# Optimization experiments

Measured on AMD Instinct MI355X. Metric: run time of the kernel, lower is better.

## Reference

```python
import jax, jax.numpy as jnp
import numpy as np

BATCH, SEQ, D_IN = 4, 2048, 1024
STATE, D_OUT, KX = 1024, 1024, 10


def setup_inputs() -> dict:
    key = jax.random.key(0)
    k0, k1, k2, k3, k4, k5 = jax.random.split(key, 6)
    inputs = jax.random.normal(k0, (BATCH, SEQ, D_IN), jnp.float32)
    h0 = jax.random.normal(k1, (STATE,), jnp.float32)
    A = jax.random.normal(k2, (STATE,), jnp.float32)
    A = A / jnp.max(jnp.abs(A))  # matches init_A / max|init_A|
    B = jax.random.normal(k3, (D_IN, STATE), jnp.float32) / D_IN
    C = jax.random.normal(k4, (STATE, D_OUT), jnp.float32) / STATE
    M = jax.random.normal(k5, (D_IN, D_OUT, KX), jnp.float32) / D_OUT
    return {"inputs": inputs, "h0": h0, "A": A, "B": B, "C": C, "M": M}


def compute_ar_x_preds(w, x):
    # w: (d_out, d_in, k); x: (b, l, d_in)
    d_out, d_in, k = w.shape
    b, l, _ = x.shape
    o = jnp.einsum('oik,bli->bklo', w, x)  # (b, k, l, d_out)
    shifts = jnp.arange(k)
    # roll slice i forward by i along the length axis
    o = jax.vmap(lambda oi, s: jnp.roll(oi, s, axis=1), in_axes=(1, 0), out_axes=1)(o, shifts)
    # triu mask: keep position t in slice i only if t >= i (causal AR)
    m = (jnp.arange(l)[None, :] >= shifts[:, None]).astype(o.dtype)  # (k, l)
    return jnp.sum(o * m[None, :, :, None], axis=1)  # (b, l, d_out)


def reference(inputs, h0, A, B, C, M):
    bsz = inputs.shape[0]
    h_init = jnp.broadcast_to(h0, (bsz, h0.shape[0]))  # h0.expand(bsz, state_dim)
    u_seq = jnp.swapaxes(inputs, 0, 1)  # (l, b, d_in)

    def step(h, u):
        h_new = A * h + u @ B  # diagonal recurrence
        return h_new, h_new

    _, hs = jax.lax.scan(step, h_init, u_seq)  # (l, b, state)
    all_h_t = jnp.swapaxes(hs, 0, 1)  # (b, l, state)
    lds_out = all_h_t @ C  # (b, l, d_out)
    ar = compute_ar_x_preds(M, inputs)
    return lds_out + ar
```

## Files before the change

### kernel.cpp

```cpp
#include <hip/hip_runtime.h>
#include <stdint.h>

typedef unsigned short u16;
typedef __attribute__((ext_vector_type(4))) float f32x4;
typedef __attribute__((ext_vector_type(8))) short s16x8;

#define BATCH 4
#define SEQ   2048
#define DIM   1024
#define KX    10
#define PAD   16
#define SEQP  (SEQ+PAD)

__device__ __forceinline__ u16 f2b(float f) {
    union { float f; uint32_t u; } v; v.f = f;
    uint32_t u = v.u + 0x7fffu + ((v.u >> 16) & 1u);
    return (u16)(u >> 16);
}
__device__ __forceinline__ float b2f(u16 h) {
    union { uint32_t u; float f; } v; v.u = ((uint32_t)h) << 16;
    return v.f;
}

__device__ __forceinline__ void llds16(const u16* g, u16* l) {
    __builtin_amdgcn_global_load_lds(
        (const __attribute__((address_space(1))) uint32_t*)g,
        (__attribute__((address_space(3))) uint32_t*)l, 16, 0, 0);
}

#define PREP_X_END  8256
#define PREP_C_END  10304
#define PREP_M_END  14400

__global__ __launch_bounds__(256) void k_prep(
    const float* __restrict__ x, const float* __restrict__ B,
    const float* __restrict__ C, const float* __restrict__ M,
    u16* __restrict__ Xpad, u16* __restrict__ Btr, u16* __restrict__ Wall)
{
    __shared__ float tile[32][33];
    const int bid = blockIdx.x, tid = threadIdx.x;

    if (bid < PREP_X_END) {
        int idx = bid * 256 + tid;
        long e = (long)idx * 4;
        int i = (int)(e & 1023);
        int row = (int)(e >> 10);
        int t = row % SEQP;
        int b = row / SEQP;
        ushort4 o;
        if (t < PAD) {
            o.x = 0; o.y = 0; o.z = 0; o.w = 0;
        } else {
            const float4 v = *(const float4*)(x + (((long)(b * SEQ + (t - PAD)) << 10) + i));
            o.x = f2b(v.x); o.y = f2b(v.y); o.z = f2b(v.z); o.w = f2b(v.w);
        }
        *(ushort4*)(Xpad + ((long)row << 10) + i) = o;
    } else if (bid < PREP_C_END) {
        const int tb = bid - PREP_X_END;
        const float* in = (tb < 1024) ? B : C;
        u16* out = (tb < 1024) ? Btr : Wall;
        int lb = tb & 1023;
        int bx = lb & 31, by = lb >> 5;
        int tx = tid & 31, ty = tid >> 5;
#pragma unroll
        for (int j = 0; j < 4; j++)
            tile[ty + j * 8][tx] = in[(long)(by * 32 + ty + j * 8) * 1024 + bx * 32 + tx];
        __syncthreads();
#pragma unroll
        for (int j = 0; j < 4; j++)
            out[(long)(bx * 32 + ty + j * 8) * 1024 + by * 32 + tx] = f2b(tile[tx][ty + j * 8]);
    } else {
        int idx = (bid - PREP_C_END) * 256 + tid;
        int o = idx >> 10, i = idx & 1023;
        const float* src = M + (long)idx * KX;
#pragma unroll
        for (int k = 0; k < KX; k++)
            Wall[((long)(k + 1) << 20) + ((long)o << 10) + i] = f2b(src[k]);
    }
}


__global__ void k_scan1(const u16* __restrict__ U, const float* __restrict__ A,
                        float* __restrict__ F) {
    int s = blockIdx.x * 256 + threadIdx.x;
    int bc = blockIdx.y;
    int b = bc >> 4, c = bc & 15;
    float a = A[s];
    const u16* u = U + (((long)(b * SEQ + c * 128)) << 10) + s;
    float f = 0.f;
#pragma unroll 8
    for (int j = 0; j < 128; j++) f = fmaf(a, f, b2f(u[(long)j << 10]));
    F[((long)bc << 10) + s] = f;
}

__global__ void k_scan2(const float* __restrict__ F, const float* __restrict__ A,
                        const float* __restrict__ h0, float* __restrict__ Carry) {
    int idx = blockIdx.x * 256 + threadIdx.x;
    int b = idx >> 10, s = idx & 1023;
    float a = A[s];
    float a128 = a;
#pragma unroll
    for (int q = 0; q < 7; q++) a128 *= a128;
    float carry = h0[s];
#pragma unroll
    for (int c = 0; c < 16; c++) {
        long off = ((long)(b * 16 + c) << 10) + s;
        Carry[off] = carry;
        carry = fmaf(a128, carry, F[off]);
    }
}

__global__ void k_scan3(u16* __restrict__ U, const float* __restrict__ A,
                        const float* __restrict__ Carry) {
    int s = blockIdx.x * 256 + threadIdx.x;
    int bc = blockIdx.y;
    int b = bc >> 4, c = bc & 15;
    float a = A[s];
    long base = (((long)(b * SEQ + c * 128)) << 10) + s;
    float h = Carry[((long)bc << 10) + s];
#pragma unroll 8
    for (int j = 0; j < 128; j++) {
        h = fmaf(a, h, b2f(U[base + ((long)j << 10)]));
        U[base + ((long)j << 10)] = f2b(h);
    }
}

__global__ __launch_bounds__(256) void k_gemm(
    void* __restrict__ outv, const u16* __restrict__ Xpad,
    const u16* __restrict__ Hbf, const u16* __restrict__ W,
    int ngroups, int use_h, int bf16_out)
{
    __shared__ u16 Asl[160 * 64];
    __shared__ u16 Wb2[2][128 * 64];

    const int tid  = threadIdx.x;
    const int wave = tid >> 6, lane = tid & 63;
    const int wm = wave >> 1, wn = wave & 1;
    const int quad = lane >> 4, l15 = lane & 15, l7 = lane & 7;

    const int col0 = blockIdx.x * 128;
    const int row0 = blockIdx.y * 128;
    const int bb = row0 >> 11;
    const long Xrow0 = (long)bb * SEQP + PAD + (row0 & (SEQ - 1));
    const long XslabBase = (Xrow0 - 16) << 10;
    const int lastg = ngroups - 1;

    f32x4 acc[4][4];
#pragma unroll
    for (int i = 0; i < 4; i++)
#pragma unroll
        for (int j = 0; j < 4; j++)
            acc[i][j] = (f32x4){0.f, 0.f, 0.f, 0.f};

    for (int k0 = 0; k0 < 1024; k0 += 64) {
#pragma unroll
        for (int q = 0; q < 5; q++) {
            int u = wave * 320 + q * 64 + lane;
            int row = u >> 3;
            int kc = (u & 7) ^ (row & 7);
            llds16(Xpad + XslabBase + ((long)row << 10) + k0 + kc * 8,
                   &Asl[(wave * 320 + q * 64) * 8]);
        }
        {
            int wsel = use_h ? 1 : 0;
            const u16* Wg = W + ((long)wsel << 20) + ((long)col0 << 10);
#pragma unroll
            for (int q = 0; q < 4; q++) {
                int u = wave * 256 + q * 64 + lane;
                int row = u >> 3;
                int kc = (u & 7) ^ (row & 7);
                llds16(Wg + ((long)row << 10) + k0 + kc * 8,
                       &Wb2[0][(wave * 256 + q * 64) * 8]);
            }
        }
        __syncthreads();

        for (int g = 0; g < ngroups; g++) {
            const bool isH = use_h && (g == lastg);
            if (isH) {
                const u16* Hb = Hbf + ((long)row0 << 10);
#pragma unroll
                for (int q = 0; q < 4; q++) {
                    int u = wave * 256 + q * 64 + lane;
                    int row = u >> 3;
                    int kc = (u & 7) ^ (row & 7);
                    llds16(Hb + ((long)row << 10) + k0 + kc * 8,
                           &Asl[(wave * 256 + q * 64) * 8]);
                }
                __syncthreads();
            }
            if (g < lastg) {
                int gn = g + 1;
                int wsel = use_h ? ((gn == lastg) ? 0 : gn + 1) : gn;
                const u16* Wg = W + ((long)wsel << 20) + ((long)col0 << 10);
                u16* dst = Wb2[gn & 1];
#pragma unroll
                for (int q = 0; q < 4; q++) {
                    int u = wave * 256 + q * 64 + lane;
                    int row = u >> 3;
                    int kc = (u & 7) ^ (row & 7);
                    llds16(Wg + ((long)row << 10) + k0 + kc * 8,
                           &dst[(wave * 256 + q * 64) * 8]);
                }
            }

            const int rbase = isH ? 0 : (16 - g);
            const int r7 = (l15 + rbase) & 7;
            const u16* Wrd = Wb2[g & 1];

            s16x8 af[4][2], bfr[4][2];
#pragma unroll
            for (int mi = 0; mi < 4; mi++) {
                int arow = rbase + wm * 64 + mi * 16 + l15;
#pragma unroll
                for (int kk = 0; kk < 2; kk++) {
                    int kca = ((kk * 4 + quad) ^ r7) << 3;
                    int kcb = ((kk * 4 + quad) ^ l7) << 3;
                    af[mi][kk]  = *(const s16x8*)&Asl[arow * 64 + kca];
                    bfr[mi][kk] = *(const s16x8*)&Wrd[(wn * 64 + mi * 16 + l15) * 64 + kcb];
                }
            }
#pragma unroll
            for (int mi = 0; mi < 4; mi++)
#pragma unroll
                for (int ni = 0; ni < 4; ni++) {
                    acc[mi][ni] = __builtin_amdgcn_mfma_f32_16x16x32_bf16(
                        af[mi][0], bfr[ni][0], acc[mi][ni], 0, 0, 0);
                    acc[mi][ni] = __builtin_amdgcn_mfma_f32_16x16x32_bf16(
                        af[mi][1], bfr[ni][1], acc[mi][ni], 0, 0, 0);
                }
            __syncthreads();
        }
    }

#pragma unroll
    for (int mi = 0; mi < 4; mi++) {
        int r = row0 + wm * 64 + mi * 16 + quad * 4;
#pragma unroll
        for (int ni = 0; ni < 4; ni++) {
            int c = col0 + wn * 64 + ni * 16 + l15;
            f32x4 v = acc[mi][ni];
            if (bf16_out) {
                u16* ob = (u16*)outv;
#pragma unroll
                for (int reg = 0; reg < 4; reg++)
                    ob[((long)(r + reg) << 10) + c] = f2b(v[reg]);
            } else {
                float* of = (float*)outv;
#pragma unroll
                for (int reg = 0; reg < 4; reg++)
                    of[((long)(r + reg) << 10) + c] = v[reg];
            }
        }
    }
}


extern "C" void kernel_launch(void* const* d_in, const int* in_sizes, int n_in,
                              void* d_out, int out_size, void* d_ws, size_t ws_size,
                              hipStream_t stream) {
    const float* x  = (const float*)d_in[0];
    const float* h0 = (const float*)d_in[1];
    const float* A  = (const float*)d_in[2];
    const float* B  = (const float*)d_in[3];
    const float* C  = (const float*)d_in[4];
    const float* M  = (const float*)d_in[5];
    float* out = (float*)d_out;

    char* ws = (char*)d_ws;
    u16*   Xpad  = (u16*)  (ws);
    u16*   Wall  = (u16*)  (ws + 16908288);
    u16*   Btr   = (u16*)  (ws + 39976960);
    u16*   Ubf   = (u16*)  (ws + 42074112);
    float* F     = (float*)(ws + 58851328);
    float* Carry = (float*)(ws + 59113472);

    k_prep<<<dim3(PREP_M_END), dim3(256), 0, stream>>>(x, B, C, M, Xpad, Btr, Wall);

    k_gemm<<<dim3(8, 64), dim3(256), 0, stream>>>(Ubf, Xpad, Ubf, Btr, 1, 0, 1);

    k_scan1<<<dim3(4, 64), dim3(256), 0, stream>>>(Ubf, A, F);
    k_scan2<<<dim3(16), dim3(256), 0, stream>>>(F, A, h0, Carry);
    k_scan3<<<dim3(4, 64), dim3(256), 0, stream>>>(Ubf, A, Carry);

    k_gemm<<<dim3(8, 64), dim3(256), 0, stream>>>(out, Xpad, Ubf, Wall, 11, 1, 0);
}
```

Before: 335.9 us.

## Triple-buffer W tiles with prefetch distance two and explicit vmcnt waits

Replaces the double-buffered W staging with a three-slot ring that prefetches the W tile two groups ahead, crossing k-block boundaries. Full __syncthreads are replaced with partial s_waitcnt vmcnt waits plus raw s_barrier, so outstanding loads can stay in flight across the MFMA phase. MFMA sections also get raised wave priority via s_setprio. This costs an extra 16KB of LDS, which may lower occupancy, and relies on hand-counted vmcnt values being correct for the async LDS loads.

```diff
diff --git a/kernel.cpp b/kernel.cpp
--- a/kernel.cpp
+++ b/kernel.cpp
@@ -27,6 +27,9 @@
         (const __attribute__((address_space(1))) uint32_t*)g,
         (__attribute__((address_space(3))) uint32_t*)l, 16, 0, 0);
 }
+
+#define WAITV4() asm volatile("s_waitcnt vmcnt(4)" ::: "memory")
+#define WAITV0() asm volatile("s_waitcnt vmcnt(0)" ::: "memory")
 
 #define PREP_X_END  8256
 #define PREP_C_END  10304
@@ -131,7 +134,7 @@
     int ngroups, int use_h, int bf16_out)
 {
     __shared__ u16 Asl[160 * 64];
-    __shared__ u16 Wb2[2][128 * 64];
+    __shared__ u16 Wb[3][128 * 64];
 
     const int tid  = threadIdx.x;
     const int wave = tid >> 6, lane = tid & 63;
@@ -152,61 +155,78 @@
         for (int j = 0; j < 4; j++)
             acc[i][j] = (f32x4){0.f, 0.f, 0.f, 0.f};
 
-    for (int k0 = 0; k0 < 1024; k0 += 64) {
+    auto stageW = [&](int k0p, int gp, int slot) {
+        int wsel = use_h ? ((gp == lastg) ? 0 : gp + 1) : gp;
+        const u16* Wg = W + ((long)wsel << 20) + ((long)col0 << 10);
+        u16* dst = &Wb[slot][0];
+#pragma unroll
+        for (int q = 0; q < 4; q++) {
+            int u = wave * 256 + q * 64 + lane;
+            int row = u >> 3;
+            int kc = (u & 7) ^ (row & 7);
+            llds16(Wg + ((long)row << 10) + k0p + kc * 8,
+                   &dst[(wave * 256 + q * 64) * 8]);
+        }
+    };
+    auto stageX = [&](int k0p) {
 #pragma unroll
         for (int q = 0; q < 5; q++) {
             int u = wave * 320 + q * 64 + lane;
             int row = u >> 3;
             int kc = (u & 7) ^ (row & 7);
-            llds16(Xpad + XslabBase + ((long)row << 10) + k0 + kc * 8,
+            llds16(Xpad + XslabBase + ((long)row << 10) + k0p + kc * 8,
                    &Asl[(wave * 320 + q * 64) * 8]);
         }
-        {
-            int wsel = use_h ? 1 : 0;
-            const u16* Wg = W + ((long)wsel << 20) + ((long)col0 << 10);
-#pragma unroll
-            for (int q = 0; q < 4; q++) {
-                int u = wave * 256 + q * 64 + lane;
-                int row = u >> 3;
-                int kc = (u & 7) ^ (row & 7);
-                llds16(Wg + ((long)row << 10) + k0 + kc * 8,
-                       &Wb2[0][(wave * 256 + q * 64) * 8]);
-            }
-        }
-        __syncthreads();
-
+    };
+    auto stageH = [&](int k0p) {
+        const u16* Hb = Hbf + ((long)row0 << 10);
+#pragma unroll
+        for (int q = 0; q < 4; q++) {
+            int u = wave * 256 + q * 64 + lane;
+            int row = u >> 3;
+            int kc = (u & 7) ^ (row & 7);
+            llds16(Hb + ((long)row << 10) + k0p + kc * 8,
+                   &Asl[(wave * 256 + q * 64) * 8]);
+        }
+    };
+
+    stageX(0);
+    stageW(0, 0, 0);
+    if (ngroups > 1) stageW(0, 1, 1);
+    else             stageW(64, 0, 1);
+    WAITV4();
+    __builtin_amdgcn_s_barrier();
+
+    int cur = 0;
+    for (int k0 = 0; k0 < 1024; k0 += 64) {
         for (int g = 0; g < ngroups; g++) {
             const bool isH = use_h && (g == lastg);
-            if (isH) {
-                const u16* Hb = Hbf + ((long)row0 << 10);
-#pragma unroll
-                for (int q = 0; q < 4; q++) {
-                    int u = wave * 256 + q * 64 + lane;
-                    int row = u >> 3;
-                    int kc = (u & 7) ^ (row & 7);
-                    llds16(Hb + ((long)row << 10) + k0 + kc * 8,
-                           &Asl[(wave * 256 + q * 64) * 8]);
-                }
-                __syncthreads();
-            }
-            if (g < lastg) {
-                int gn = g + 1;
-                int wsel = use_h ? ((gn == lastg) ? 0 : gn + 1) : gn;
-                const u16* Wg = W + ((long)wsel << 20) + ((long)col0 << 10);
-                u16* dst = Wb2[gn & 1];
-#pragma unroll
-                for (int q = 0; q < 4; q++) {
-                    int u = wave * 256 + q * 64 + lane;
-                    int row = u >> 3;
-                    int kc = (u & 7) ^ (row & 7);
-                    llds16(Wg + ((long)row << 10) + k0 + kc * 8,
-                           &dst[(wave * 256 + q * 64) * 8]);
+
+            bool restage = false;
+            if (isH)                     { stageH(k0); restage = true; }
+            else if (g == 0 && k0 > 0)   { stageX(k0); restage = true; }
+
+            bool pf = false;
+            {
+                int t = g + 2, k0p = k0, gp;
+                if (t < ngroups)              gp = t;
+                else if (t < 2 * ngroups)   { gp = t - ngroups;     k0p += 64; }
+                else                        { gp = t - 2 * ngroups; k0p += 128; }
+                if (k0p < 1024) {
+                    int slot2 = cur + 2; if (slot2 >= 3) slot2 -= 3;
+                    stageW(k0p, gp, slot2);
+                    pf = true;
                 }
             }
 
+            if (restage) {
+                if (pf) WAITV4(); else WAITV0();
+                __builtin_amdgcn_s_barrier();
+            }
+
             const int rbase = isH ? 0 : (16 - g);
             const int r7 = (l15 + rbase) & 7;
-            const u16* Wrd = Wb2[g & 1];
+            const u16* Wrd = &Wb[cur][0];
 
             s16x8 af[4][2], bfr[4][2];
 #pragma unroll
@@ -220,6 +240,7 @@
                     bfr[mi][kk] = *(const s16x8*)&Wrd[(wn * 64 + mi * 16 + l15) * 64 + kcb];
                 }
             }
+            __builtin_amdgcn_s_setprio(1);
 #pragma unroll
             for (int mi = 0; mi < 4; mi++)
 #pragma unroll
@@ -229,7 +250,11 @@
                     acc[mi][ni] = __builtin_amdgcn_mfma_f32_16x16x32_bf16(
                         af[mi][1], bfr[ni][1], acc[mi][ni], 0, 0, 0);
                 }
-            __syncthreads();
+            __builtin_amdgcn_s_setprio(0);
+
+            if (pf) WAITV4(); else WAITV0();
+            __builtin_amdgcn_s_barrier();
+            cur = cur + 1; if (cur >= 3) cur -= 3;
         }
     }
 
```

New measurement: 348.4 us. 1.04x slower.

## Add 8-wave final GEMM reusing shifted X slab across AR taps

Applied to the files above, without the earlier changes.

Replaces the final fused AR+LDS GEMM with a new 512-thread kernel that uses 256-row tiles. For each K chunk it loads one X slab of 265 rows into LDS and reuses it for all 10 shifted AR taps by offsetting the row base, restaging only for the H operand. Weight tiles are triple-buffered with a two-step prefetch, and s_setprio is raised around the MFMA bursts. The goal is to cut redundant global and LDS loads of X and to hide weight-load latency. The cost is higher LDS use per block, fewer blocks in the grid, and more barriers per step.

```diff
diff --git a/kernel.cpp b/kernel.cpp
--- a/kernel.cpp
+++ b/kernel.cpp
@@ -255,6 +255,182 @@
     }
 }
 
+__global__ __launch_bounds__(512) void k_gemm8(
+    float* __restrict__ out, const u16* __restrict__ Xpad,
+    const u16* __restrict__ Hbf, const u16* __restrict__ W)
+{
+    __shared__ u16 Asl[272 * 64];
+    __shared__ u16 Wb[3][128 * 64];
+
+    const int tid  = threadIdx.x;
+    const int wave = tid >> 6, lane = tid & 63;
+    const int wm = wave >> 1, wn = wave & 1;
+    const int quad = lane >> 4, l15 = lane & 15, l7 = lane & 7;
+
+    const int col0 = blockIdx.x * 128;
+    const int row0 = blockIdx.y * 256;
+    const int bb = row0 >> 11;
+    const long Xrow0 = (long)bb * SEQP + PAD + (row0 & (SEQ - 1));
+    const long XslabBase = (Xrow0 - 9) << 10;
+
+    f32x4 acc[4][4];
+#pragma unroll
+    for (int i = 0; i < 4; i++)
+#pragma unroll
+        for (int j = 0; j < 4; j++)
+            acc[i][j] = (f32x4){0.f, 0.f, 0.f, 0.f};
+
+    auto stageW = [&](int k0p, int wsel, int slot, int part) {
+        const u16* Wg = W + ((long)wsel << 20) + ((long)col0 << 10);
+        int u = part * 512 + tid;
+        int row = u >> 3;
+        int kc = (u & 7) ^ (row & 7);
+        llds16(Wg + ((long)row << 10) + k0p + kc * 8,
+               &Wb[slot][(part * 512 + wave * 64) * 8]);
+    };
+    auto stageX = [&](int k0p) {
+#pragma unroll
+        for (int q = 0; q < 4; q++) {
+            int u = wave * 272 + q * 64 + lane;
+            int row = u >> 3;
+            int kc = (u & 7) ^ (row & 7);
+            llds16(Xpad + XslabBase + ((long)row << 10) + k0p + kc * 8,
+                   &Asl[(wave * 272 + q * 64) * 8]);
+        }
+        {
+            int u = wave * 272 + 256 + lane;
+            int row = u >> 3;
+            int kc = (u & 7) ^ (row & 7);
+            if (lane < 16)
+                llds16(Xpad + XslabBase + ((long)row << 10) + k0p + kc * 8,
+                       &Asl[(wave * 272 + 256) * 8]);
+        }
+    };
+    auto stageH = [&](int k0p) {
+        const u16* Hb = Hbf + ((long)row0 << 10);
+#pragma unroll
+        for (int q = 0; q < 4; q++) {
+            int u = q * 512 + tid;
+            int row = u >> 3;
+            int kc = (u & 7) ^ (row & 7);
+            llds16(Hb + ((long)row << 10) + k0p + kc * 8,
+                   &Asl[(q * 512 + wave * 64) * 8]);
+        }
+    };
+
+    stageX(0);
+    stageW(0, 1, 0, 0); stageW(0, 1, 0, 1);
+    stageW(0, 2, 1, 0); stageW(0, 2, 1, 1);
+    asm volatile("s_waitcnt vmcnt(2)" ::: "memory");
+    __builtin_amdgcn_s_barrier();
+
+    int slot = 0;
+    for (int kk0 = 0; kk0 < 16; ++kk0) {
+        const int k0 = kk0 * 64;
+        for (int g = 0; g < 11; ++g) {
+            const bool isH = (g == 10);
+            const bool restage = isH || (g == 0 && kk0 > 0);
+
+            int g2 = g + 2, kk2 = kk0;
+            if (g2 >= 11) { g2 -= 11; kk2 += 1; }
+            const bool pf = (kk2 < 16);
+            const int wsel2 = (g2 == 10) ? 0 : (g2 + 1);
+            const int slot2 = (slot + 2 >= 3) ? slot + 2 - 3 : slot + 2;
+
+            if (isH)           stageH(k0);
+            else if (restage)  stageX(k0);
+
+            if (pf) stageW(kk2 * 64, wsel2, slot2, 0);
+
+            if (restage) {
+                if (pf) asm volatile("s_waitcnt vmcnt(1)" ::: "memory");
+                else    asm volatile("s_waitcnt vmcnt(0)" ::: "memory");
+                __builtin_amdgcn_s_barrier();
+            }
+
+            const int rbase = isH ? 0 : (9 - g);
+            const u16* Wrd = &Wb[slot][0];
+
+            s16x8 bfr[4][2], af[2][2];
+#pragma unroll
+            for (int ni = 0; ni < 4; ni++) {
+                int brow = wn * 64 + ni * 16 + l15;
+#pragma unroll
+                for (int kk = 0; kk < 2; kk++) {
+                    int kcb = ((kk * 4 + quad) ^ l7) << 3;
+                    bfr[ni][kk] = *(const s16x8*)&Wrd[brow * 64 + kcb];
+                }
+            }
+#pragma unroll
+            for (int i = 0; i < 2; i++) {
+                int arow = rbase + wm * 64 + i * 16 + l15;
+                int r7 = arow & 7;
+#pragma unroll
+                for (int kk = 0; kk < 2; kk++) {
+                    int kca = ((kk * 4 + quad) ^ r7) << 3;
+                    af[i][kk] = *(const s16x8*)&Asl[arow * 64 + kca];
+                }
+            }
+            __builtin_amdgcn_s_barrier();
+            __builtin_amdgcn_s_setprio(1);
+#pragma unroll
+            for (int i = 0; i < 2; i++)
+#pragma unroll
+                for (int ni = 0; ni < 4; ni++) {
+                    acc[i][ni] = __builtin_amdgcn_mfma_f32_16x16x32_bf16(
+                        af[i][0], bfr[ni][0], acc[i][ni], 0, 0, 0);
+                    acc[i][ni] = __builtin_amdgcn_mfma_f32_16x16x32_bf16(
+                        af[i][1], bfr[ni][1], acc[i][ni], 0, 0, 0);
+                }
+            __builtin_amdgcn_s_setprio(0);
+            __builtin_amdgcn_s_barrier();
+
+            s16x8 af2[2][2];
+#pragma unroll
+            for (int i = 0; i < 2; i++) {
+                int arow = rbase + wm * 64 + (i + 2) * 16 + l15;
+                int r7 = arow & 7;
+#pragma unroll
+                for (int kk = 0; kk < 2; kk++) {
+                    int kca = ((kk * 4 + quad) ^ r7) << 3;
+                    af2[i][kk] = *(const s16x8*)&Asl[arow * 64 + kca];
+                }
+            }
+            if (pf) stageW(kk2 * 64, wsel2, slot2, 1);
+            __builtin_amdgcn_s_barrier();
+            __builtin_amdgcn_s_setprio(1);
+#pragma unroll
+            for (int i = 0; i < 2; i++)
+#pragma unroll
+                for (int ni = 0; ni < 4; ni++) {
+                    acc[i + 2][ni] = __builtin_amdgcn_mfma_f32_16x16x32_bf16(
+                        af2[i][0], bfr[ni][0], acc[i + 2][ni], 0, 0, 0);
+                    acc[i + 2][ni] = __builtin_amdgcn_mfma_f32_16x16x32_bf16(
+                        af2[i][1], bfr[ni][1], acc[i + 2][ni], 0, 0, 0);
+                }
+            __builtin_amdgcn_s_setprio(0);
+            if (pf) asm volatile("s_waitcnt vmcnt(2)" ::: "memory");
+            else    asm volatile("s_waitcnt vmcnt(0)" ::: "memory");
+            __builtin_amdgcn_s_barrier();
+
+            slot = (slot == 2) ? 0 : slot + 1;
+        }
+    }
+
+#pragma unroll
+    for (int mi = 0; mi < 4; mi++) {
+        int r = row0 + wm * 64 + mi * 16 + quad * 4;
+#pragma unroll
+        for (int ni = 0; ni < 4; ni++) {
+            int c = col0 + wn * 64 + ni * 16 + l15;
+            f32x4 v = acc[mi][ni];
+#pragma unroll
+            for (int reg = 0; reg < 4; reg++)
+                out[((long)(r + reg) << 10) + c] = v[reg];
+        }
+    }
+}
+
 
 extern "C" void kernel_launch(void* const* d_in, const int* in_sizes, int n_in,
                               void* d_out, int out_size, void* d_ws, size_t ws_size,
@@ -283,5 +459,5 @@
     k_scan2<<<dim3(16), dim3(256), 0, stream>>>(F, A, h0, Carry);
     k_scan3<<<dim3(4, 64), dim3(256), 0, stream>>>(Ubf, A, Carry);
 
-    k_gemm<<<dim3(8, 64), dim3(256), 0, stream>>>(out, Xpad, Ubf, Wall, 11, 1, 0);
-}
+    k_gemm8<<<dim3(8, 32), dim3(512), 0, stream>>>(out, Xpad, Ubf, Wall);
+}
```

Result: slower. 379.1 us (+12.9%).
